# Optimization experiments

Measured on AMD Instinct MI355X. Metric: run time of the kernel, lower is better.

The kernel has to match this reference:

```python
import jax, jax.numpy as jnp
import numpy as np

D_MODEL = 192   # embed_dim
DEPTH = 24
D_INNER = 384   # expand=2 * d_model
D_STATE = 16
D_CONV = 4
DT_RANK = 12    # ceil(192/16)
B = 8
IMG = 224
P = 16          # patch size / stride


def setup_inputs() -> dict:
    key = jax.random.key(0)
    ks = jax.random.split(key, 10)
    s = lambda k, shp, sc=0.02: jax.random.normal(k, shp, jnp.float32) * sc
    return {
        "x": jax.random.normal(ks[0], (B, 3, IMG, IMG), jnp.float32),
        "pe_w": s(ks[1], (D_MODEL, 3, P, P)),
        "pe_b": jnp.zeros((D_MODEL,), jnp.float32),
        "norm_w": jnp.ones((DEPTH, D_MODEL), jnp.float32),
        "norm_b": jnp.zeros((DEPTH, D_MODEL), jnp.float32),
        "in_proj_w": s(ks[2], (DEPTH, 2 * D_INNER, D_MODEL)),
        "conv_w": s(ks[3], (DEPTH, D_INNER, D_CONV), 0.1),
        "conv_b": jnp.zeros((DEPTH, D_INNER), jnp.float32),
        "xproj_w": s(ks[4], (DEPTH, DT_RANK + 2 * D_STATE, D_INNER)),
        "dtproj_w": s(ks[5], (DEPTH, D_INNER, DT_RANK), 0.1),
        "dtproj_b": s(ks[6], (DEPTH, D_INNER), 0.1),
        "A_log": jnp.broadcast_to(jnp.log(jnp.arange(1.0, D_STATE + 1.0, dtype=jnp.float32)), (DEPTH, D_INNER, D_STATE)).astype(jnp.float32),
        "D_param": jnp.ones((DEPTH, D_INNER), jnp.float32),
        "outproj_w": s(ks[7], (DEPTH, D_MODEL, D_INNER)),
        "normf_w": jnp.ones((D_MODEL,), jnp.float32),
        "normf_b": jnp.zeros((D_MODEL,), jnp.float32),
    }


def _layernorm(x, w, b, eps=1e-5):
    mu = x.mean(-1, keepdims=True)
    var = ((x - mu) ** 2).mean(-1, keepdims=True)
    return (x - mu) * jax.lax.rsqrt(var + eps) * w + b


def _causal_dwconv(x, w, b):
    # x: [B, L, d_inner]; depthwise causal conv1d (mamba conv1d, padding=d_conv-1, truncated to L)
    xt = jnp.pad(x.swapaxes(1, 2), ((0, 0), (0, 0), (D_CONV - 1, 0)))  # [B, di, L+3]
    y = jax.lax.conv_general_dilated(xt, w[:, None, :], (1,), 'VALID',
                                     feature_group_count=w.shape[0])
    return (y + b[:, None]).swapaxes(1, 2)  # [B, L, di]


def _selective_scan(u, dt, Bm, Cm, A, Dp):
    # u, dt: [B, L, di]; Bm, Cm: [B, L, ds]; A: [di, ds]; Dp: [di]
    dA = jnp.exp(dt[..., None] * A)                         # [B, L, di, ds]
    dBu = (dt * u)[..., None] * Bm[:, :, None, :]           # [B, L, di, ds]

    def step(h, inp):
        dA_t, dBu_t, C_t = inp
        h = dA_t * h + dBu_t                                # [B, di, ds]
        return h, jnp.einsum('bds,bs->bd', h, C_t)

    h0 = jnp.zeros((u.shape[0], A.shape[0], A.shape[1]), u.dtype)
    _, ys = jax.lax.scan(step, h0,
                         (dA.swapaxes(0, 1), dBu.swapaxes(0, 1), Cm.swapaxes(0, 1)))
    return ys.swapaxes(0, 1) + u * Dp                       # [B, L, di]


def _mamba(x, ipw, cw, cb, xpw, dtw, dtb, Alog, Dp, opw):
    xz = jnp.einsum('bld,ed->ble', x, ipw)                  # [B, L, 2*di]
    xin, z = jnp.split(xz, 2, axis=-1)
    xin = jax.nn.silu(_causal_dwconv(xin, cw, cb))
    xdbl = jnp.einsum('bld,ed->ble', xin, xpw)              # [B, L, dt_rank+2*ds]
    dt = jax.nn.softplus(jnp.einsum('blr,dr->bld', xdbl[..., :DT_RANK], dtw) + dtb)
    Bm = xdbl[..., DT_RANK:DT_RANK + D_STATE]
    Cm = xdbl[..., DT_RANK + D_STATE:]
    A = -jnp.exp(Alog)
    y = _selective_scan(xin, dt, Bm, Cm, A, Dp)
    y = y * jax.nn.silu(z)
    return jnp.einsum('bld,ed->ble', y, opw)                # [B, L, D]


def reference(x, pe_w, pe_b, norm_w, norm_b, in_proj_w, conv_w, conv_b,
              xproj_w, dtproj_w, dtproj_b, A_log, D_param, outproj_w,
              normf_w, normf_b):
    # PatchEmbed: conv stride 16 -> flatten -> [B, 196, 192]
    feat = jax.lax.conv_general_dilated(x, pe_w, (P, P), 'VALID') + pe_b[None, :, None, None]
    h = feat.reshape(feat.shape[0], D_MODEL, -1).swapaxes(1, 2)
    residual = None
    for i in range(DEPTH):
        residual = h if residual is None else residual + h
        hn = _layernorm(residual, norm_w[i], norm_b[i])
        h = _mamba(hn, in_proj_w[i], conv_w[i], conv_b[i], xproj_w[i],
                   dtproj_w[i], dtproj_b[i], A_log[i], D_param[i], outproj_w[i])
    residual = residual + h
    return _layernorm(residual, normf_w, normf_b)           # [B, 196, 192]
```

## Files before the change

kernel.cpp:

```cpp
#include <hip/hip_runtime.h>
#include <hip/hip_bf16.h>


#define NTOK   1568
#define DMODEL 192
#define DINNER 384
#define DSTATE 16
#define DTRANK 12
#define DEPTH  24
#define LSEQ   196
#define TCH    49

typedef __attribute__((ext_vector_type(8))) short short8;
typedef __attribute__((ext_vector_type(4))) float floatx4;

__device__ inline short f2bf(float f) {
    __hip_bfloat16 h = __float2bfloat16(f);
    return *reinterpret_cast<short*>(&h);
}

__global__ __launch_bounds__(256) void im2col(
    const float* __restrict__ x, float* __restrict__ patches)
{
    int idx = blockIdx.x * 256 + threadIdx.x;
    if (idx >= NTOK * 768) return;
    int tok = idx / 768, e = idx % 768;
    int b = tok / LSEQ, l = tok % LSEQ;
    int py = l / 14, px = l % 14;
    int ic = e >> 8, rem = e & 255, ky = rem >> 4, kx = rem & 15;
    patches[idx] = x[((b * 3 + ic) * 224 + py * 16 + ky) * 224 + px * 16 + kx];
}

#define LDA 40
__global__ __launch_bounds__(256) void gemm_bf16(
    const float* __restrict__ A, const float* __restrict__ W,
    const float* __restrict__ bias, float* __restrict__ C,
    int M, int N, int K)
{
    __shared__ short As[64 * LDA];
    __shared__ short Ws[64 * LDA];
    int tid = threadIdx.x;
    int m0 = blockIdx.x * 64, n0 = blockIdx.y * 64;
    int wv = tid >> 6, lane = tid & 63;
    int fm = lane & 15, q = lane >> 4;
    int row = tid >> 2, kc = (tid & 3) * 8;
    floatx4 acc[4] = {{0.f,0.f,0.f,0.f},{0.f,0.f,0.f,0.f},{0.f,0.f,0.f,0.f},{0.f,0.f,0.f,0.f}};

    for (int k0 = 0; k0 < K; k0 += 32) {
        {
            int m = m0 + row;
            float4 a0 = make_float4(0.f,0.f,0.f,0.f), a1 = a0;
            if (m < M) {
                a0 = *(const float4*)&A[(size_t)m * K + k0 + kc];
                a1 = *(const float4*)&A[(size_t)m * K + k0 + kc + 4];
            }
            short8 v;
            v[0]=f2bf(a0.x); v[1]=f2bf(a0.y); v[2]=f2bf(a0.z); v[3]=f2bf(a0.w);
            v[4]=f2bf(a1.x); v[5]=f2bf(a1.y); v[6]=f2bf(a1.z); v[7]=f2bf(a1.w);
            *(short8*)&As[row * LDA + kc] = v;
        }
        {
            int n = n0 + row;
            float4 b0 = *(const float4*)&W[(size_t)n * K + k0 + kc];
            float4 b1 = *(const float4*)&W[(size_t)n * K + k0 + kc + 4];
            short8 v;
            v[0]=f2bf(b0.x); v[1]=f2bf(b0.y); v[2]=f2bf(b0.z); v[3]=f2bf(b0.w);
            v[4]=f2bf(b1.x); v[5]=f2bf(b1.y); v[6]=f2bf(b1.z); v[7]=f2bf(b1.w);
            *(short8*)&Ws[row * LDA + kc] = v;
        }
        __syncthreads();
        short8 af = *(const short8*)&As[(wv * 16 + fm) * LDA + q * 8];
#pragma unroll
        for (int nt = 0; nt < 4; ++nt) {
            short8 bf = *(const short8*)&Ws[(nt * 16 + fm) * LDA + q * 8];
            acc[nt] = __builtin_amdgcn_mfma_f32_16x16x32_bf16(af, bf, acc[nt], 0, 0, 0);
        }
        __syncthreads();
    }
#pragma unroll
    for (int nt = 0; nt < 4; ++nt) {
        int col = n0 + nt * 16 + fm;
        float bv = bias ? bias[col] : 0.f;
#pragma unroll
        for (int r = 0; r < 4; ++r) {
            int mrow = m0 + wv * 16 + q * 4 + r;
            if (mrow < M) C[(size_t)mrow * N + col] = acc[nt][r] + bv;
        }
    }
}

__global__ __launch_bounds__(64) void addln(
    const float* __restrict__ h, float* __restrict__ residual,
    float* __restrict__ out, const float* __restrict__ w,
    const float* __restrict__ b, int addH)
{
    int t = blockIdx.x;
    int lane = threadIdx.x;
    int base = t * DMODEL;
    float v[3];
#pragma unroll
    for (int i = 0; i < 3; ++i) {
        int c = lane + i * 64;
        float r = residual[base + c];
        if (addH) r += h[base + c];
        v[i] = r;
        residual[base + c] = r;
    }
    float s = v[0] + v[1] + v[2];
#pragma unroll
    for (int o = 32; o >= 1; o >>= 1) s += __shfl_xor(s, o);
    float mean = s * (1.0f / DMODEL);
    float q = 0.f;
#pragma unroll
    for (int i = 0; i < 3; ++i) { float d = v[i] - mean; q += d * d; }
#pragma unroll
    for (int o = 32; o >= 1; o >>= 1) q += __shfl_xor(q, o);
    float rstd = rsqrtf(q * (1.0f / DMODEL) + 1e-5f);
#pragma unroll
    for (int i = 0; i < 3; ++i) {
        int c = lane + i * 64;
        out[base + c] = (v[i] - mean) * rstd * w[c] + b[c];
    }
}

__global__ __launch_bounds__(256) void conv_xproj_dt(
    const float* __restrict__ xz, const float* __restrict__ cw,
    const float* __restrict__ cb, const float* __restrict__ xpw,
    const float* __restrict__ dtw, const float* __restrict__ dtb,
    float* __restrict__ u, float* __restrict__ dtg, float* __restrict__ bcg)
{
    __shared__ float su[DINNER];
    __shared__ float sx[44];
    int blk = blockIdx.x;
    int b = blk / LSEQ, l = blk % LSEQ;
    int tid = threadIdx.x;
    for (int d = tid; d < DINNER; d += 256) {
        float acc = cb[d];
#pragma unroll
        for (int k = 0; k < 4; ++k) {
            int li = l - 3 + k;
            if (li >= 0) acc += xz[(size_t)(b * LSEQ + li) * 768 + d] * cw[d * 4 + k];
        }
        float sig = 1.f / (1.f + __expf(-acc));
        float val = acc * sig;
        su[d] = val;
        u[(size_t)(b * LSEQ + l) * DINNER + d] = val;
    }
    __syncthreads();
    if (tid < 176) {
        int e = tid >> 2, p = tid & 3;
        float acc = 0.f;
        const float* wr = &xpw[e * DINNER + p * 96];
        const float* ur = &su[p * 96];
#pragma unroll 8
        for (int j = 0; j < 96; ++j) acc += ur[j] * wr[j];
        acc += __shfl_xor(acc, 1);
        acc += __shfl_xor(acc, 2);
        if (p == 0) sx[e] = acc;
    }
    __syncthreads();
    for (int d = tid; d < DINNER; d += 256) {
        float acc = dtb[d];
#pragma unroll
        for (int r = 0; r < DTRANK; ++r) acc += sx[r] * dtw[d * DTRANK + r];
        float sp = (acc > 20.f) ? acc : log1pf(__expf(acc));
        dtg[(size_t)(b * LSEQ + l) * DINNER + d] = sp;
    }
    if (tid < 32) bcg[(b * LSEQ + l) * 32 + tid] = sx[DTRANK + tid];
}

#define SPAD 272
__global__ __launch_bounds__(256) void scan_kernel(
    const float* __restrict__ u, const float* __restrict__ dtg,
    const float* __restrict__ bc, const float* __restrict__ xz,
    const float* __restrict__ Alog, const float* __restrict__ Dp,
    float* __restrict__ y)
{
    __shared__ float sdt[TCH][16];
    __shared__ float su_[TCH][16];
    __shared__ float sz_[TCH][16];
    __shared__ float sB_[TCH][16];
    __shared__ float sC_[TCH][16];
    __shared__ float sprod[TCH][SPAD];

    int b  = blockIdx.x / 24;
    int dg = blockIdx.x % 24;
    int tid = threadIdx.x;
    int s = tid & 15, dl = tid >> 4;
    int d = dg * 16 + dl;
    float Ads = -expf(Alog[d * DSTATE + s]);
    float Dd2 = Dp[dg * 16 + (tid & 15)];
    float h = 0.f;

    for (int c0 = 0; c0 < LSEQ; c0 += TCH) {
        if (tid < TCH * 4) {
            int t = tid >> 2, j4 = (tid & 3) * 4;
            size_t tok = (size_t)(b * LSEQ + c0 + t);
            *(float4*)&sdt[t][j4] = *(const float4*)&dtg[tok * DINNER + dg * 16 + j4];
            *(float4*)&su_[t][j4] = *(const float4*)&u  [tok * DINNER + dg * 16 + j4];
            *(float4*)&sz_[t][j4] = *(const float4*)&xz [tok * 768 + DINNER + dg * 16 + j4];
            *(float4*)&sB_[t][j4] = *(const float4*)&bc [tok * 32 + j4];
            *(float4*)&sC_[t][j4] = *(const float4*)&bc [tok * 32 + 16 + j4];
        }
        __syncthreads();

#pragma unroll 7
        for (int t = 0; t < TCH; ++t) {
            float dtv = sdt[t][dl];
            float uv  = su_[t][dl];
            float Bv  = sB_[t][s];
            float Cv  = sC_[t][s];
            float dA  = __expf(dtv * Ads);
            h = dA * h + (dtv * uv) * Bv;
            sprod[t][dl * 17 + s] = h * Cv;
        }
        __syncthreads();

        for (int i = tid; i < TCH * 16; i += 256) {
            int t = i >> 4, dl2 = i & 15;
            float sum = 0.f;
#pragma unroll
            for (int j = 0; j < 16; ++j) sum += sprod[t][dl2 * 17 + j];
            float uv = su_[t][dl2];
            float zv = sz_[t][dl2];
            float sig = 1.f / (1.f + __expf(-zv));
            y[(size_t)(b * LSEQ + c0 + t) * DINNER + dg * 16 + dl2] =
                (sum + uv * Dd2) * (zv * sig);
        }
        __syncthreads();
    }
}

extern "C" void kernel_launch(void* const* d_in, const int* in_sizes, int n_in,
                              void* d_out, int out_size, void* d_ws, size_t ws_size,
                              hipStream_t stream)
{
    const float* x         = (const float*)d_in[0];
    const float* pe_w      = (const float*)d_in[1];
    const float* pe_b      = (const float*)d_in[2];
    const float* norm_w    = (const float*)d_in[3];
    const float* norm_b    = (const float*)d_in[4];
    const float* in_proj_w = (const float*)d_in[5];
    const float* conv_w    = (const float*)d_in[6];
    const float* conv_b    = (const float*)d_in[7];
    const float* xproj_w   = (const float*)d_in[8];
    const float* dtproj_w  = (const float*)d_in[9];
    const float* dtproj_b  = (const float*)d_in[10];
    const float* A_log     = (const float*)d_in[11];
    const float* D_param   = (const float*)d_in[12];
    const float* outproj_w = (const float*)d_in[13];
    const float* normf_w   = (const float*)d_in[14];
    const float* normf_b   = (const float*)d_in[15];

    float* ws = (float*)d_ws;
    float* residual = ws;
    float* hn       = residual + 301056;
    float* hbuf     = hn + 301056;
    float* xz       = hbuf + 301056;
    float* ubuf     = xz + 1204224;
    float* dtbuf    = ubuf + 602112;
    float* ybuf     = dtbuf + 602112;
    float* bcbuf    = ybuf + 602112;
    float* patches  = ubuf;

    im2col<<<(NTOK * 768 + 255) / 256, 256, 0, stream>>>(x, patches);
    gemm_bf16<<<dim3(25, 3), 256, 0, stream>>>(
        patches, pe_w, pe_b, residual, NTOK, DMODEL, 768);

    for (int i = 0; i < DEPTH; ++i) {
        addln<<<NTOK, 64, 0, stream>>>(hbuf, residual, hn,
                                       norm_w + i * DMODEL, norm_b + i * DMODEL,
                                       i > 0 ? 1 : 0);
        gemm_bf16<<<dim3(25, 12), 256, 0, stream>>>(
            hn, in_proj_w + (size_t)i * 768 * DMODEL, nullptr, xz, NTOK, 768, DMODEL);
        conv_xproj_dt<<<NTOK, 256, 0, stream>>>(
            xz, conv_w + (size_t)i * DINNER * 4, conv_b + (size_t)i * DINNER,
            xproj_w + (size_t)i * 44 * DINNER, dtproj_w + (size_t)i * DINNER * DTRANK,
            dtproj_b + (size_t)i * DINNER, ubuf, dtbuf, bcbuf);
        scan_kernel<<<192, 256, 0, stream>>>(
            ubuf, dtbuf, bcbuf, xz, A_log + (size_t)i * DINNER * DSTATE,
            D_param + (size_t)i * DINNER, ybuf);
        gemm_bf16<<<dim3(25, 3), 256, 0, stream>>>(
            ybuf, outproj_w + (size_t)i * DMODEL * DINNER, nullptr, hbuf, NTOK, DMODEL, DINNER);
    }

    addln<<<NTOK, 64, 0, stream>>>(hbuf, residual, (float*)d_out,
                                   normf_w, normf_b, 1);
}
```

Measured before the change: 1.672 ms.

## Fuse residual add and LayerNorm into out-proj GEMM epilogue, pass bf16 activations

```diff
diff --git a/kernel.cpp b/kernel.cpp
--- a/kernel.cpp
+++ b/kernel.cpp
@@ -20,7 +20,7 @@
 }
 
 __global__ __launch_bounds__(256) void im2col(
-    const float* __restrict__ x, float* __restrict__ patches)
+    const float* __restrict__ x, __hip_bfloat16* __restrict__ patches)
 {
     int idx = blockIdx.x * 256 + threadIdx.x;
     if (idx >= NTOK * 768) return;
@@ -28,14 +28,14 @@
     int b = tok / LSEQ, l = tok % LSEQ;
     int py = l / 14, px = l % 14;
     int ic = e >> 8, rem = e & 255, ky = rem >> 4, kx = rem & 15;
-    patches[idx] = x[((b * 3 + ic) * 224 + py * 16 + ky) * 224 + px * 16 + kx];
+    patches[idx] = __float2bfloat16(x[((b * 3 + ic) * 224 + py * 16 + ky) * 224 + px * 16 + kx]);
 }
 
 #define LDA 40
-__global__ __launch_bounds__(256) void gemm_bf16(
-    const float* __restrict__ A, const float* __restrict__ W,
-    const float* __restrict__ bias, float* __restrict__ C,
-    int M, int N, int K)
+
+__global__ __launch_bounds__(256) void gemm_in(
+    const __hip_bfloat16* __restrict__ A, const float* __restrict__ W,
+    float* __restrict__ C, int M, int N, int K)
 {
     __shared__ short As[64 * LDA];
     __shared__ short Ws[64 * LDA];
@@ -44,19 +44,15 @@
     int wv = tid >> 6, lane = tid & 63;
     int fm = lane & 15, q = lane >> 4;
     int row = tid >> 2, kc = (tid & 3) * 8;
-    floatx4 acc[4] = {{0.f,0.f,0.f,0.f},{0.f,0.f,0.f,0.f},{0.f,0.f,0.f,0.f},{0.f,0.f,0.f,0.f}};
+    floatx4 acc[4];
+#pragma unroll
+    for (int nt = 0; nt < 4; ++nt) acc[nt] = (floatx4){0.f, 0.f, 0.f, 0.f};
 
     for (int k0 = 0; k0 < K; k0 += 32) {
         {
             int m = m0 + row;
-            float4 a0 = make_float4(0.f,0.f,0.f,0.f), a1 = a0;
-            if (m < M) {
-                a0 = *(const float4*)&A[(size_t)m * K + k0 + kc];
-                a1 = *(const float4*)&A[(size_t)m * K + k0 + kc + 4];
-            }
-            short8 v;
-            v[0]=f2bf(a0.x); v[1]=f2bf(a0.y); v[2]=f2bf(a0.z); v[3]=f2bf(a0.w);
-            v[4]=f2bf(a1.x); v[5]=f2bf(a1.y); v[6]=f2bf(a1.z); v[7]=f2bf(a1.w);
+            short8 v = {0,0,0,0,0,0,0,0};
+            if (m < M) v = *(const short8*)&A[(size_t)m * K + k0 + kc];
             *(short8*)&As[row * LDA + kc] = v;
         }
         {
@@ -80,46 +76,102 @@
 #pragma unroll
     for (int nt = 0; nt < 4; ++nt) {
         int col = n0 + nt * 16 + fm;
-        float bv = bias ? bias[col] : 0.f;
 #pragma unroll
         for (int r = 0; r < 4; ++r) {
             int mrow = m0 + wv * 16 + q * 4 + r;
-            if (mrow < M) C[(size_t)mrow * N + col] = acc[nt][r] + bv;
-        }
-    }
-}
-
-__global__ __launch_bounds__(64) void addln(
-    const float* __restrict__ h, float* __restrict__ residual,
-    float* __restrict__ out, const float* __restrict__ w,
-    const float* __restrict__ b, int addH)
-{
-    int t = blockIdx.x;
-    int lane = threadIdx.x;
-    int base = t * DMODEL;
-    float v[3];
-#pragma unroll
-    for (int i = 0; i < 3; ++i) {
-        int c = lane + i * 64;
-        float r = residual[base + c];
-        if (addH) r += h[base + c];
-        v[i] = r;
-        residual[base + c] = r;
-    }
-    float s = v[0] + v[1] + v[2];
-#pragma unroll
-    for (int o = 32; o >= 1; o >>= 1) s += __shfl_xor(s, o);
-    float mean = s * (1.0f / DMODEL);
-    float q = 0.f;
-#pragma unroll
-    for (int i = 0; i < 3; ++i) { float d = v[i] - mean; q += d * d; }
-#pragma unroll
-    for (int o = 32; o >= 1; o >>= 1) q += __shfl_xor(q, o);
-    float rstd = rsqrtf(q * (1.0f / DMODEL) + 1e-5f);
-#pragma unroll
-    for (int i = 0; i < 3; ++i) {
-        int c = lane + i * 64;
-        out[base + c] = (v[i] - mean) * rstd * w[c] + b[c];
+            if (mrow < M) C[(size_t)mrow * N + col] = acc[nt][r];
+        }
+    }
+}
+
+__global__ __launch_bounds__(256) void gemm_ln(
+    const __hip_bfloat16* __restrict__ A, const float* __restrict__ W,
+    const float* __restrict__ bias, float* __restrict__ residual,
+    __hip_bfloat16* __restrict__ hn, float* __restrict__ outf,
+    const float* __restrict__ lnw, const float* __restrict__ lnb,
+    int M, int K, int accumulate)
+{
+    __shared__ short As[64 * LDA];
+    __shared__ short Ws[192 * LDA];
+    __shared__ float slw[192], slb[192], sbias[192];
+    int tid = threadIdx.x;
+    int m0 = blockIdx.x * 64;
+    int wv = tid >> 6, lane = tid & 63;
+    int fm = lane & 15, q = lane >> 4;
+    int row = tid >> 2, kc = (tid & 3) * 8;
+    if (tid < 192) {
+        slw[tid] = lnw[tid];
+        slb[tid] = lnb[tid];
+        sbias[tid] = bias ? bias[tid] : 0.f;
+    }
+    floatx4 acc[12];
+#pragma unroll
+    for (int nt = 0; nt < 12; ++nt) acc[nt] = (floatx4){0.f, 0.f, 0.f, 0.f};
+
+    for (int k0 = 0; k0 < K; k0 += 32) {
+        {
+            int m = m0 + row;
+            short8 v = {0,0,0,0,0,0,0,0};
+            if (m < M) v = *(const short8*)&A[(size_t)m * K + k0 + kc];
+            *(short8*)&As[row * LDA + kc] = v;
+        }
+#pragma unroll
+        for (int j = 0; j < 3; ++j) {
+            int n = row + 64 * j;
+            float4 b0 = *(const float4*)&W[(size_t)n * K + k0 + kc];
+            float4 b1 = *(const float4*)&W[(size_t)n * K + k0 + kc + 4];
+            short8 v;
+            v[0]=f2bf(b0.x); v[1]=f2bf(b0.y); v[2]=f2bf(b0.z); v[3]=f2bf(b0.w);
+            v[4]=f2bf(b1.x); v[5]=f2bf(b1.y); v[6]=f2bf(b1.z); v[7]=f2bf(b1.w);
+            *(short8*)&Ws[n * LDA + kc] = v;
+        }
+        __syncthreads();
+        short8 af = *(const short8*)&As[(wv * 16 + fm) * LDA + q * 8];
+#pragma unroll
+        for (int nt = 0; nt < 12; ++nt) {
+            short8 bf = *(const short8*)&Ws[(nt * 16 + fm) * LDA + q * 8];
+            acc[nt] = __builtin_amdgcn_mfma_f32_16x16x32_bf16(af, bf, acc[nt], 0, 0, 0);
+        }
+        __syncthreads();
+    }
+
+#pragma unroll
+    for (int r = 0; r < 4; ++r) {
+        int m = m0 + wv * 16 + q * 4 + r;
+        bool valid = m < M;
+        float v[12];
+        float sum = 0.f;
+#pragma unroll
+        for (int nt = 0; nt < 12; ++nt) {
+            int col = nt * 16 + fm;
+            float t = acc[nt][r] + sbias[col];
+            if (accumulate && valid) t += residual[(size_t)m * DMODEL + col];
+            v[nt] = t;
+            sum += t;
+        }
+        if (valid) {
+#pragma unroll
+            for (int nt = 0; nt < 12; ++nt)
+                residual[(size_t)m * DMODEL + nt * 16 + fm] = v[nt];
+        }
+        sum += __shfl_xor(sum, 1); sum += __shfl_xor(sum, 2);
+        sum += __shfl_xor(sum, 4); sum += __shfl_xor(sum, 8);
+        float mean = sum * (1.f / DMODEL);
+        float sq = 0.f;
+#pragma unroll
+        for (int nt = 0; nt < 12; ++nt) { float d = v[nt] - mean; sq += d * d; }
+        sq += __shfl_xor(sq, 1); sq += __shfl_xor(sq, 2);
+        sq += __shfl_xor(sq, 4); sq += __shfl_xor(sq, 8);
+        float rstd = rsqrtf(sq * (1.f / DMODEL) + 1e-5f);
+        if (valid) {
+#pragma unroll
+            for (int nt = 0; nt < 12; ++nt) {
+                int col = nt * 16 + fm;
+                float o = (v[nt] - mean) * rstd * slw[col] + slb[col];
+                if (outf) outf[(size_t)m * DMODEL + col] = o;
+                else      hn[(size_t)m * DMODEL + col] = __float2bfloat16(o);
+            }
+        }
     }
 }
 
@@ -174,7 +226,7 @@
     const float* __restrict__ u, const float* __restrict__ dtg,
     const float* __restrict__ bc, const float* __restrict__ xz,
     const float* __restrict__ Alog, const float* __restrict__ Dp,
-    float* __restrict__ y)
+    __hip_bfloat16* __restrict__ y)
 {
     __shared__ float sdt[TCH][16];
     __shared__ float su_[TCH][16];
@@ -225,7 +277,7 @@
             float zv = sz_[t][dl2];
             float sig = 1.f / (1.f + __expf(-zv));
             y[(size_t)(b * LSEQ + c0 + t) * DINNER + dg * 16 + dl2] =
-                (sum + uv * Dd2) * (zv * sig);
+                __float2bfloat16((sum + uv * Dd2) * (zv * sig));
         }
         __syncthreads();
     }
@@ -254,36 +306,35 @@
 
     float* ws = (float*)d_ws;
     float* residual = ws;
-    float* hn       = residual + 301056;
-    float* hbuf     = hn + 301056;
-    float* xz       = hbuf + 301056;
+    float* xz       = residual + 301056;
     float* ubuf     = xz + 1204224;
     float* dtbuf    = ubuf + 602112;
-    float* ybuf     = dtbuf + 602112;
-    float* bcbuf    = ybuf + 602112;
-    float* patches  = ubuf;
+    float* bcbuf    = dtbuf + 602112;
+    __hip_bfloat16* hn  = (__hip_bfloat16*)(bcbuf + 50176);
+    __hip_bfloat16* ybf = hn + 301056;
+    __hip_bfloat16* patches = (__hip_bfloat16*)ubuf;
 
     im2col<<<(NTOK * 768 + 255) / 256, 256, 0, stream>>>(x, patches);
-    gemm_bf16<<<dim3(25, 3), 256, 0, stream>>>(
-        patches, pe_w, pe_b, residual, NTOK, DMODEL, 768);
+    gemm_ln<<<25, 256, 0, stream>>>(
+        patches, pe_w, pe_b, residual, hn, nullptr,
+        norm_w, norm_b, NTOK, 768, 0);
 
     for (int i = 0; i < DEPTH; ++i) {
-        addln<<<NTOK, 64, 0, stream>>>(hbuf, residual, hn,
-                                       norm_w + i * DMODEL, norm_b + i * DMODEL,
-                                       i > 0 ? 1 : 0);
-        gemm_bf16<<<dim3(25, 12), 256, 0, stream>>>(
-            hn, in_proj_w + (size_t)i * 768 * DMODEL, nullptr, xz, NTOK, 768, DMODEL);
+        int last = (i == DEPTH - 1);
+        gemm_in<<<dim3(25, 12), 256, 0, stream>>>(
+            hn, in_proj_w + (size_t)i * 768 * DMODEL, xz, NTOK, 768, DMODEL);
         conv_xproj_dt<<<NTOK, 256, 0, stream>>>(
             xz, conv_w + (size_t)i * DINNER * 4, conv_b + (size_t)i * DINNER,
             xproj_w + (size_t)i * 44 * DINNER, dtproj_w + (size_t)i * DINNER * DTRANK,
             dtproj_b + (size_t)i * DINNER, ubuf, dtbuf, bcbuf);
         scan_kernel<<<192, 256, 0, stream>>>(
             ubuf, dtbuf, bcbuf, xz, A_log + (size_t)i * DINNER * DSTATE,
-            D_param + (size_t)i * DINNER, ybuf);
-        gemm_bf16<<<dim3(25, 3), 256, 0, stream>>>(
-            ybuf, outproj_w + (size_t)i * DMODEL * DINNER, nullptr, hbuf, NTOK, DMODEL, DINNER);
-    }
-
-    addln<<<NTOK, 64, 0, stream>>>(hbuf, residual, (float*)d_out,
-                                   normf_w, normf_b, 1);
-}
+            D_param + (size_t)i * DINNER, ybf);
+        gemm_ln<<<25, 256, 0, stream>>>(
+            ybf, outproj_w + (size_t)i * DMODEL * DINNER, nullptr, residual, hn,
+            last ? (float*)d_out : nullptr,
+            last ? normf_w : norm_w + (i + 1) * DMODEL,
+            last ? normf_b : norm_b + (i + 1) * DMODEL,
+            NTOK, DINNER, 1);
+    }
+}
```

New measurement: 1.904 ms. 13.8% more time.
